# Optimization experiments

Hardware: AMD Instinct MI355X
Metric: run time of the kernel (lower is better)

Reference implementation:

```python
import jax, jax.numpy as jnp
import numpy as np

RADIUS = 0.1
NSAMPLE = 32


def setup_inputs() -> dict:
    key = jax.random.key(0)
    k1, k2, k3 = jax.random.split(key, 3)
    B, N, P, C = 2, 16384, 4096, 64
    xyz = jax.random.uniform(k1, (B, N, 3), dtype=jnp.float32)
    new_xyz = jax.random.uniform(k2, (B, P, 3), dtype=jnp.float32)
    features = jax.random.normal(k3, (B, C, N), dtype=jnp.float32)
    return {"xyz": xyz, "new_xyz": new_xyz, "features": features}


def _ball_query(xyz, new_xyz, radius, nsample):
    """Return (B, npoint, nsample) int32 indices of the first `nsample` points
    (in original order) within `radius` of each query center. Slots beyond the
    number of valid neighbors are padded with the first valid index (0 if none),
    matching the standard PointNet++ CUDA ball_query semantics."""
    N = xyz.shape[1]
    # squared distances [B, P, N]
    d2 = jnp.sum((new_xyz[:, :, None, :] - xyz[:, None, :, :]) ** 2, axis=-1)
    in_ball = d2 < (radius * radius)
    # score = point index if in ball, else N (sentinel); smallest nsample scores
    # are the first nsample in-ball indices in original order.
    score = jnp.where(in_ball, jnp.arange(N, dtype=jnp.int32), jnp.int32(N))
    neg_topk, _ = jax.lax.top_k(-score, nsample)  # largest of -score == smallest score
    idx = -neg_topk  # [B, P, nsample], ascending
    first = idx[..., :1]
    idx = jnp.where(idx >= N, first, idx)  # pad invalid slots with first valid
    idx = jnp.where(idx >= N, 0, idx)      # no neighbor at all -> 0
    return idx


def _group(features, idx):
    """features (B, C, N), idx (B, P, S) -> (B, C, P, S)"""
    return jax.vmap(lambda f, i: f[:, i])(features, idx)


def reference(xyz, new_xyz, features):
    idx = _ball_query(xyz, new_xyz, RADIUS, NSAMPLE)          # (B, P, S)
    xyz_t = jnp.transpose(xyz, (0, 2, 1))                      # (B, 3, N)
    grouped_xyz = _group(xyz_t, idx)                           # (B, 3, P, S)
    grouped_xyz = grouped_xyz - jnp.transpose(new_xyz, (0, 2, 1))[..., None]
    grouped_features = _group(features, idx)                   # (B, C, P, S)
    new_features = jnp.concatenate([grouped_xyz, grouped_features], axis=1)
    return new_features
```

## Files before the change

kernel.cpp:

```cpp
#include <hip/hip_runtime.h>
#include <limits.h>

#define BB 2
#define NN 16384
#define PP 4096
#define CC 64
#define SS 32
#define R2 0.01f
#define OUTCH (3 + CC)
#define GRES 10
#define NCELL 1000
#define TILE 128

__device__ __forceinline__ int cell_of(float v) {
  int q = (int)(v * 10.0f);
  return q < 0 ? 0 : (q > GRES - 1 ? GRES - 1 : q);
}
__device__ __forceinline__ int cell_clamp_floor(float v) {
  int q = (int)floorf(v * 10.0f);
  return q < 0 ? 0 : (q > GRES - 1 ? GRES - 1 : q);
}

__global__ __launch_bounds__(1024) void bin_kernel(
    const float* __restrict__ xyz, int* __restrict__ cellStartG,
    float4* __restrict__ sorted4) {
  __shared__ int hist[NCELL];
  __shared__ int fill[NCELL];
  __shared__ int cstart[NCELL];
  __shared__ int wtot[16];
  const int b = blockIdx.x;
  const int t = threadIdx.x;
  const int lane = t & 63;
  const int w = t >> 6;

  if (t < NCELL) { hist[t] = 0; fill[t] = 0; }
  __syncthreads();

  const float* __restrict__ xb = xyz + (size_t)b * NN * 3;
  int cells[16];
#pragma unroll
  for (int k = 0; k < 16; ++k) {
    const int i = t + k * 1024;
    const float x = xb[i * 3 + 0];
    const float y = xb[i * 3 + 1];
    const float z = xb[i * 3 + 2];
    const int c = (cell_of(z) * GRES + cell_of(y)) * GRES + cell_of(x);
    cells[k] = c;
    atomicAdd(&hist[c], 1);
  }
  __syncthreads();

  const int own = (t < NCELL) ? hist[t] : 0;
  int incl = own;
#pragma unroll
  for (int d = 1; d < 64; d <<= 1) {
    const int v = __shfl_up(incl, d);
    if (lane >= d) incl += v;
  }
  if (lane == 63) wtot[w] = incl;
  __syncthreads();
  int pre = 0;
#pragma unroll
  for (int k = 0; k < 16; ++k) pre += (k < w) ? wtot[k] : 0;
  const int excl = pre + incl - own;
  if (t < NCELL) {
    cstart[t] = excl;
    cellStartG[b * 1001 + t] = excl;
  }
  if (t == 0) cellStartG[b * 1001 + NCELL] = NN;
  __syncthreads();

#pragma unroll
  for (int k = 0; k < 16; ++k) {
    const int i = t + k * 1024;
    const float x = xb[i * 3 + 0];
    const float y = xb[i * 3 + 1];
    const float z = xb[i * 3 + 2];
    const int c = cells[k];
    const int r = atomicAdd(&fill[c], 1);
    float4 v;
    v.x = x; v.y = y; v.z = z; v.w = __int_as_float(i);
    sorted4[(size_t)b * NN + cstart[c] + r] = v;
  }
}

__global__ __launch_bounds__(256) void transpose_feat_kernel(
    const float* __restrict__ feat, float* __restrict__ featT) {
  __shared__ float tile[64][65];
  const int n0 = blockIdx.x * 64;
  const int b = blockIdx.y;
  const int jn = threadIdx.x & 63;
  const int g4 = threadIdx.x >> 6;

  const float* fb = feat + (size_t)b * CC * NN;
#pragma unroll
  for (int k = 0; k < 16; ++k) {
    const int c = g4 * 16 + k;
    tile[c][jn] = fb[(size_t)c * NN + n0 + jn];
  }
  __syncthreads();
  float* ft = featT + ((size_t)b * NN + n0) * CC;
#pragma unroll
  for (int k = 0; k < 16; ++k) {
    const int j = g4 * 16 + k;
    ft[(size_t)j * CC + jn] = tile[jn][j];
  }
}

__global__ __launch_bounds__(256) void query_group_kernel(
    const float4* __restrict__ sorted4, const int* __restrict__ cellStart,
    const float* __restrict__ new_xyz, const float* __restrict__ xyz,
    const float* __restrict__ featT, float* __restrict__ out) {
#pragma clang fp contract(off)
  __shared__ float smem[TILE * 65];
  __shared__ int idxsm[TILE];
  const int widx = threadIdx.x >> 6;
  const int lane = threadIdx.x & 63;
  const int wave = blockIdx.x * 4 + widx;
  const int b = wave >> 12;
  unsigned* bm = (unsigned*)smem + widx * 576;
  int* myout = idxsm + widx * SS;

  const float cx = new_xyz[wave * 3 + 0];
  const float cy = new_xyz[wave * 3 + 1];
  const float cz = new_xyz[wave * 3 + 2];
  const float4* __restrict__ sb = sorted4 + (size_t)b * NN;
  const int* __restrict__ csb = cellStart + b * 1001;

#pragma unroll
  for (int k = 0; k < 9; ++k) bm[k * 64 + lane] = 0;

  const float mg = 0.1f + 1e-5f;
  const int lox = cell_clamp_floor(cx - mg), hix = cell_clamp_floor(cx + mg);
  const int loy = cell_clamp_floor(cy - mg), hiy = cell_clamp_floor(cy + mg);
  const int loz = cell_clamp_floor(cz - mg), hiz = cell_clamp_floor(cz + mg);
  const int nx = hix - lox + 1;
  const int ny = hiy - loy + 1;
  const int nz = hiz - loz + 1;
  const int nr = nz * ny;

  int s_l = 0, len_l = 0;
  if (lane < nr) {
    int zi, yi;
    if (ny == 1) { zi = lane; yi = 0; }
    else if (ny == 2) { zi = lane >> 1; yi = lane & 1; }
    else { zi = (lane * 11) >> 5; yi = lane - zi * 3; }
    const int c0 = ((loz + zi) * GRES + (loy + yi)) * GRES + lox;
    s_l = csb[c0];
    len_l = csb[c0 + nx] - s_l;
  }
  int incl = len_l;
#pragma unroll
  for (int d = 1; d <= 8; d <<= 1) {
    const int v = __shfl_up(incl, d);
    if (lane >= d) incl += v;
  }
  const int T = __shfl(incl, nr - 1);
  const int Lx = incl - len_l;

  int Lk[9], Sk[9];
#pragma unroll
  for (int k = 0; k < 9; ++k) {
    Lk[k] = __shfl(Lx, k);
    Sk[k] = __shfl(s_l, k);
  }

  for (int t0 = 0; t0 < T; t0 += 64) {
    const int g = t0 + lane;
    if (g < T) {
      int L = Lk[0], S = Sk[0];
#pragma unroll
      for (int k = 1; k < 9; ++k) {
        const bool cge = g >= Lk[k];
        L = cge ? Lk[k] : L;
        S = cge ? Sk[k] : S;
      }
      const float4 pt = sb[S + (g - L)];
      const float dx = cx - pt.x;
      const float dy = cy - pt.y;
      const float dz = cz - pt.z;
      const float a = dx * dx + dy * dy;
      const float d2 = a + dz * dz;
      if (d2 < R2) {
        const int orig = __float_as_int(pt.w);
        const int wi = orig >> 5;
        atomicOr(&bm[(wi >> 3) * 9 + (wi & 7)], 1u << (orig & 31));
      }
    }
  }
  __threadfence_block();

  unsigned wv[8];
  int c = 0;
  int fi = INT_MAX;
#pragma unroll
  for (int k = 0; k < 8; ++k) {
    wv[k] = bm[lane * 9 + k];
    c += (int)__popc(wv[k]);
    if (fi == INT_MAX && wv[k])
      fi = lane * 256 + k * 32 + (int)__builtin_ctz(wv[k]);
  }

  int incl2 = c;
#pragma unroll
  for (int d = 1; d < 64; d <<= 1) {
    const int t = __shfl_up(incl2, d);
    if (lane >= d) incl2 += t;
  }
  const int E = incl2 - c;
  const int total = __shfl(incl2, 63);

  const unsigned long long nb = __ballot(c > 0);
  int fc = 0;
  if (nb) fc = __shfl(fi, (int)__builtin_ctzll(nb));

  int s = E;
  if (s < SS) {
#pragma unroll
    for (int k = 0; k < 8; ++k) {
      unsigned ww = wv[k];
      while (ww && s < SS) {
        const int bpos = (int)__builtin_ctz(ww);
        ww &= ww - 1;
        myout[s++] = lane * 256 + k * 32 + bpos;
      }
      if (s >= SS) break;
    }
  }
  for (int s2 = total + lane; s2 < SS; s2 += 64) myout[s2] = fc;

  __syncthreads();

  const int base = blockIdx.x * TILE;
  const int t = threadIdx.x;
  const size_t PS = (size_t)PP * SS;

  const float4* ftb = (const float4*)(featT + (size_t)b * NN * CC);
#pragma unroll
  for (int k = 0; k < 8; ++k) {
    const int u = k * 256 + t;
    const int r = u >> 4;
    const int q = u & 15;
    const int v = idxsm[r];
    const float4 val = ftb[(size_t)v * 16 + q];
    float* dst = &smem[r * 65 + q * 4];
    dst[0] = val.x; dst[1] = val.y; dst[2] = val.z; dst[3] = val.w;
  }
  __syncthreads();

  if (t < TILE) {
    const int g = base + t;
    const int v = idxsm[t];
    const int p = (g >> 5) & (PP - 1);
    const float* xr = xyz + ((size_t)b * NN + v) * 3;
    const float* cr = new_xyz + (size_t)(b * PP + p) * 3;
    const size_t ob = (size_t)b * OUTCH * PS + ((size_t)g & (PS - 1));
    out[ob + 0 * PS] = xr[0] - cr[0];
    out[ob + 1 * PS] = xr[1] - cr[1];
    out[ob + 2 * PS] = xr[2] - cr[2];
  }

  float* ob3 = out + (size_t)b * OUTCH * PS + 3 * PS + ((size_t)base & (PS - 1));
#pragma unroll
  for (int k = 0; k < 32; ++k) {
    const int u = k * 256 + t;
    const int c2 = u >> 7;
    const int r = u & 127;
    ob3[(size_t)c2 * PS + r] = smem[r * 65 + c2];
  }
}

extern "C" void kernel_launch(void* const* d_in, const int* in_sizes, int n_in,
                              void* d_out, int out_size, void* d_ws, size_t ws_size,
                              hipStream_t stream) {
  const float* xyz = (const float*)d_in[0];
  const float* new_xyz = (const float*)d_in[1];
  const float* feat = (const float*)d_in[2];
  float* out = (float*)d_out;

  float* featT = (float*)d_ws;
  const size_t featTBytes = (size_t)BB * NN * CC * sizeof(float);
  float4* sorted4 = (float4*)((char*)d_ws + featTBytes);
  int* cellStart = (int*)((char*)d_ws + featTBytes + (size_t)BB * NN * sizeof(float4));

  bin_kernel<<<BB, 1024, 0, stream>>>(xyz, cellStart, sorted4);
  transpose_feat_kernel<<<dim3(NN / 64, BB), 256, 0, stream>>>(feat, featT);
  query_group_kernel<<<(BB * PP) / 4, 256, 0, stream>>>(sorted4, cellStart,
                                                        new_xyz, xyz, featT, out);
}
```

Before: 61.06 us.

## Split binning into parallel kernels, prune x-range per row, prefetch candidate points

The single two-block binning kernel becomes a memset plus three grid-wide kernels: a global-atomic histogram, a per-batch scan, and a scatter. This spreads work that previously ran on only two workgroups across the GPU, at the cost of extra launches and global atomics. In the query kernel, each y/z cell row now narrows its x cell range using the minimum y/z distance to the row, so fewer candidate points are scanned. The candidate loop also software-prefetches the next point while testing the current one. Because the scatter order within a cell is nondeterministic, sorted order changes, but the bitmask selection keeps the output correct.

```diff
diff --git a/kernel.cpp b/kernel.cpp
--- a/kernel.cpp
+++ b/kernel.cpp
@@ -21,67 +21,46 @@
   return q < 0 ? 0 : (q > GRES - 1 ? GRES - 1 : q);
 }
 
-__global__ __launch_bounds__(1024) void bin_kernel(
-    const float* __restrict__ xyz, int* __restrict__ cellStartG,
-    float4* __restrict__ sorted4) {
-  __shared__ int hist[NCELL];
-  __shared__ int fill[NCELL];
-  __shared__ int cstart[NCELL];
-  __shared__ int wtot[16];
+__global__ __launch_bounds__(256) void hist_kernel(const float* __restrict__ xyz,
+                                                   int* __restrict__ hist) {
+  const int i = blockIdx.x * 256 + threadIdx.x;
+  const int b = i >> 14;
+  const float* p = xyz + (size_t)i * 3;
+  const int c = (cell_of(p[2]) * GRES + cell_of(p[1])) * GRES + cell_of(p[0]);
+  atomicAdd(hist + b * NCELL + c, 1);
+}
+
+__global__ __launch_bounds__(1024) void scan_kernel(const int* __restrict__ hist,
+                                                    int* __restrict__ cellStart) {
+  __shared__ int sm[1024];
   const int b = blockIdx.x;
   const int t = threadIdx.x;
-  const int lane = t & 63;
-  const int w = t >> 6;
-
-  if (t < NCELL) { hist[t] = 0; fill[t] = 0; }
-  __syncthreads();
-
-  const float* __restrict__ xb = xyz + (size_t)b * NN * 3;
-  int cells[16];
-#pragma unroll
-  for (int k = 0; k < 16; ++k) {
-    const int i = t + k * 1024;
-    const float x = xb[i * 3 + 0];
-    const float y = xb[i * 3 + 1];
-    const float z = xb[i * 3 + 2];
-    const int c = (cell_of(z) * GRES + cell_of(y)) * GRES + cell_of(x);
-    cells[k] = c;
-    atomicAdd(&hist[c], 1);
-  }
-  __syncthreads();
-
-  const int own = (t < NCELL) ? hist[t] : 0;
-  int incl = own;
-#pragma unroll
-  for (int d = 1; d < 64; d <<= 1) {
-    const int v = __shfl_up(incl, d);
-    if (lane >= d) incl += v;
-  }
-  if (lane == 63) wtot[w] = incl;
-  __syncthreads();
-  int pre = 0;
-#pragma unroll
-  for (int k = 0; k < 16; ++k) pre += (k < w) ? wtot[k] : 0;
-  const int excl = pre + incl - own;
-  if (t < NCELL) {
-    cstart[t] = excl;
-    cellStartG[b * 1001 + t] = excl;
-  }
-  if (t == 0) cellStartG[b * 1001 + NCELL] = NN;
-  __syncthreads();
-
-#pragma unroll
-  for (int k = 0; k < 16; ++k) {
-    const int i = t + k * 1024;
-    const float x = xb[i * 3 + 0];
-    const float y = xb[i * 3 + 1];
-    const float z = xb[i * 3 + 2];
-    const int c = cells[k];
-    const int r = atomicAdd(&fill[c], 1);
-    float4 v;
-    v.x = x; v.y = y; v.z = z; v.w = __int_as_float(i);
-    sorted4[(size_t)b * NN + cstart[c] + r] = v;
-  }
+  const int own = (t < NCELL) ? hist[b * NCELL + t] : 0;
+  sm[t] = own;
+  __syncthreads();
+  for (int off = 1; off < 1024; off <<= 1) {
+    const int v = (t >= off) ? sm[t - off] : 0;
+    __syncthreads();
+    sm[t] += v;
+    __syncthreads();
+  }
+  if (t < NCELL) cellStart[b * 1001 + t] = sm[t] - own;
+  if (t == NCELL - 1) cellStart[b * 1001 + NCELL] = sm[t];
+}
+
+__global__ __launch_bounds__(256) void scatter_kernel(
+    const float* __restrict__ xyz, const int* __restrict__ cellStart,
+    int* __restrict__ fill, float4* __restrict__ sorted4) {
+  const int i = blockIdx.x * 256 + threadIdx.x;
+  const int b = i >> 14;
+  const float* p = xyz + (size_t)i * 3;
+  const float x = p[0], y = p[1], z = p[2];
+  const int c = (cell_of(z) * GRES + cell_of(y)) * GRES + cell_of(x);
+  const int r = atomicAdd(fill + b * NCELL + c, 1);
+  const int pos = cellStart[b * 1001 + c] + r;
+  float4 v;
+  v.x = x; v.y = y; v.z = z; v.w = __int_as_float(i & (NN - 1));
+  sorted4[(size_t)b * NN + pos] = v;
 }
 
 __global__ __launch_bounds__(256) void transpose_feat_kernel(
@@ -131,10 +110,8 @@
   for (int k = 0; k < 9; ++k) bm[k * 64 + lane] = 0;
 
   const float mg = 0.1f + 1e-5f;
-  const int lox = cell_clamp_floor(cx - mg), hix = cell_clamp_floor(cx + mg);
   const int loy = cell_clamp_floor(cy - mg), hiy = cell_clamp_floor(cy + mg);
   const int loz = cell_clamp_floor(cz - mg), hiz = cell_clamp_floor(cz + mg);
-  const int nx = hix - lox + 1;
   const int ny = hiy - loy + 1;
   const int nz = hiz - loz + 1;
   const int nr = nz * ny;
@@ -145,9 +122,19 @@
     if (ny == 1) { zi = lane; yi = 0; }
     else if (ny == 2) { zi = lane >> 1; yi = lane & 1; }
     else { zi = (lane * 11) >> 5; yi = lane - zi * 3; }
-    const int c0 = ((loz + zi) * GRES + (loy + yi)) * GRES + lox;
-    s_l = csb[c0];
-    len_l = csb[c0 + nx] - s_l;
+    const int zc = loz + zi, yc = loy + yi;
+    const float y0 = yc * 0.1f, z0 = zc * 0.1f;
+    const float dymin = fmaxf(fmaxf(y0 - cy, cy - (y0 + 0.1f)), 0.0f);
+    const float dzmin = fmaxf(fmaxf(z0 - cz, cz - (z0 + 0.1f)), 0.0f);
+    const float rem = mg * mg - dymin * dymin - dzmin * dzmin;
+    if (rem > 0.0f) {
+      const float dxa = sqrtf(rem) * 1.0000002f + 1e-7f;
+      const int lxr = cell_clamp_floor(cx - dxa);
+      const int hxr = cell_clamp_floor(cx + dxa);
+      const int c0 = (zc * GRES + yc) * GRES + lxr;
+      s_l = csb[c0];
+      len_l = csb[c0 + (hxr - lxr + 1)] - s_l;
+    }
   }
   int incl = len_l;
 #pragma unroll
@@ -165,28 +152,38 @@
     Sk[k] = __shfl(s_l, k);
   }
 
-  for (int t0 = 0; t0 < T; t0 += 64) {
-    const int g = t0 + lane;
+  auto flat_load = [&](int g) -> float4 {
+    int L = Lk[0], S = Sk[0];
+#pragma unroll
+    for (int k = 1; k < 9; ++k) {
+      const bool cge = g >= Lk[k];
+      L = cge ? Lk[k] : L;
+      S = cge ? Sk[k] : S;
+    }
+    return sb[S + (g - L)];
+  };
+
+  const int nIt = (T + 63) >> 6;
+  float4 cur = {};
+  if (lane < T) cur = flat_load(lane);
+  for (int it = 0; it < nIt; ++it) {
+    float4 nxt = cur;
+    const int gn = (it + 1) * 64 + lane;
+    if (gn < T) nxt = flat_load(gn);
+    const int g = it * 64 + lane;
     if (g < T) {
-      int L = Lk[0], S = Sk[0];
-#pragma unroll
-      for (int k = 1; k < 9; ++k) {
-        const bool cge = g >= Lk[k];
-        L = cge ? Lk[k] : L;
-        S = cge ? Sk[k] : S;
-      }
-      const float4 pt = sb[S + (g - L)];
-      const float dx = cx - pt.x;
-      const float dy = cy - pt.y;
-      const float dz = cz - pt.z;
+      const float dx = cx - cur.x;
+      const float dy = cy - cur.y;
+      const float dz = cz - cur.z;
       const float a = dx * dx + dy * dy;
       const float d2 = a + dz * dz;
       if (d2 < R2) {
-        const int orig = __float_as_int(pt.w);
+        const int orig = __float_as_int(cur.w);
         const int wi = orig >> 5;
         atomicOr(&bm[(wi >> 3) * 9 + (wi & 7)], 1u << (orig & 31));
       }
     }
+    cur = nxt;
   }
   __threadfence_block();
 
@@ -279,11 +276,18 @@
   float* out = (float*)d_out;
 
   float* featT = (float*)d_ws;
-  const size_t featTBytes = (size_t)BB * NN * CC * sizeof(float);
-  float4* sorted4 = (float4*)((char*)d_ws + featTBytes);
-  int* cellStart = (int*)((char*)d_ws + featTBytes + (size_t)BB * NN * sizeof(float4));
-
-  bin_kernel<<<BB, 1024, 0, stream>>>(xyz, cellStart, sorted4);
+  char* p = (char*)d_ws + (size_t)BB * NN * CC * sizeof(float);
+  float4* sorted4 = (float4*)p;
+  p += (size_t)BB * NN * sizeof(float4);
+  int* cellStart = (int*)p;
+  p += (size_t)BB * 1001 * sizeof(int);
+  int* hist = (int*)p;
+  int* fill = hist + BB * NCELL;
+
+  hipMemsetAsync(hist, 0, (size_t)2 * BB * NCELL * sizeof(int), stream);
+  hist_kernel<<<(BB * NN) / 256, 256, 0, stream>>>(xyz, hist);
+  scan_kernel<<<BB, 1024, 0, stream>>>(hist, cellStart);
+  scatter_kernel<<<(BB * NN) / 256, 256, 0, stream>>>(xyz, cellStart, fill, sorted4);
   transpose_feat_kernel<<<dim3(NN / 64, BB), 256, 0, stream>>>(feat, featT);
   query_group_kernel<<<(BB * PP) / 4, 256, 0, stream>>>(sorted4, cellStart,
                                                         new_xyz, xyz, featT, out);
```

After: 66.27 us. 8.5% more time.
